# Performance work log

Hardware: AMD Instinct MI355X
Metric: run time of the kernel (lower is better)

The kernel has to match this reference:

```python
import jax, jax.numpy as jnp
import numpy as np

NUM_SKILLS = 300
EMB_SIZE = 256
CURVE_DIM = 64  # splits: 21 / 21 / 22
B, S = 512, 200


def setup_inputs() -> dict:
    key = jax.random.key(0)
    ks = jax.random.split(key, 11)
    d3 = CURVE_DIM // 3
    dm = d3 + CURVE_DIM % 3
    return {
        "q": jax.random.randint(ks[0], (B, S), 0, NUM_SKILLS, dtype=jnp.int32),
        "r": jax.random.randint(ks[1], (B, S), 0, 2, dtype=jnp.int32),
        "qry": jax.random.randint(ks[2], (B, S), 0, NUM_SKILLS, dtype=jnp.int32),
        "skill_w": jax.random.normal(ks[3], (d3,), jnp.float32),
        "skill_b": jax.random.normal(ks[4], (d3,), jnp.float32),
        "att_w": jax.random.normal(ks[5], (d3,), jnp.float32),
        "att_b": jax.random.normal(ks[6], (d3,), jnp.float32),
        "mast_w": jax.random.normal(ks[7], (dm,), jnp.float32),
        "mast_b": jax.random.normal(ks[8], (dm,), jnp.float32),
        "proj_w": jax.random.normal(ks[9], (EMB_SIZE, CURVE_DIM), jnp.float32) * 0.05,
        "proj_b": jax.random.normal(ks[10], (EMB_SIZE,), jnp.float32),
    }


def _running_counts(q, r):
    """Per-(b,t) running attempt count and correct count for the skill at (b,t).
    Returns attempts[B,S], correct[B,S] (float32), valid[B,S] (bool)."""
    b, s = q.shape
    rows = jnp.arange(b)
    valid = (q >= 0) & (q < NUM_SKILLS)
    idx = jnp.clip(q, 0, NUM_SKILLS - 1)

    def step(carry, xs):
        att, cor = carry  # [B, NUM_SKILLS] int32
        it, rt, vt = xs   # [B] each
        att = att.at[rows, it].add(vt.astype(jnp.int32))
        cor = cor.at[rows, it].add((rt * vt).astype(jnp.int32))
        return (att, cor), (att[rows, it], cor[rows, it])

    init = (jnp.zeros((b, NUM_SKILLS), jnp.int32), jnp.zeros((b, NUM_SKILLS), jnp.int32))
    xs = (idx.T, r.T, valid.T)  # scan over time
    _, (a_t, c_t) = jax.lax.scan(step, init, xs)
    return a_t.T.astype(jnp.float32), c_t.T.astype(jnp.float32), valid


def reference(q, r, qry, skill_w, skill_b, att_w, att_b, mast_w, mast_b, proj_w, proj_b):
    attempts, correct, valid = _running_counts(q, r)  # [B,S]
    mastery = correct / jnp.maximum(attempts, 1.0)
    skill_f = q.astype(jnp.float32)
    # Linear(1, d): scalar * w + b, broadcast over [B,S]
    s_enc = skill_f[..., None] * skill_w + skill_b        # [B,S,21]
    n_enc = attempts[..., None] * att_w + att_b           # [B,S,21]
    m_enc = mastery[..., None] * mast_w + mast_b          # [B,S,22]
    tup = jnp.concatenate([s_enc, n_enc, m_enc], axis=-1)  # [B,S,CURVE_DIM]
    traj = jnp.einsum('bsc,ec->bse', tup, proj_w) + proj_b  # [B,S,EMB]
    return jnp.where(valid[..., None], traj, 0.0)
```

## Files before the change

### kernel.cpp

```cpp
#include <hip/hip_runtime.h>

constexpr int NUM_SKILLS = 300;
constexpr int EMB = 256;
constexpr int CD  = 64;
constexpr int D3  = 21;
constexpr int DM  = 22;
constexpr int SEQ = 200;

__global__ __launch_bounds__(256)
void traj_enc_kernel(const int* __restrict__ q, const int* __restrict__ r,
                     const float* __restrict__ skill_w, const float* __restrict__ skill_b,
                     const float* __restrict__ att_w,   const float* __restrict__ att_b,
                     const float* __restrict__ mast_w,  const float* __restrict__ mast_b,
                     const float* __restrict__ proj_w,  const float* __restrict__ proj_b,
                     float* __restrict__ out)
{
    __shared__ __align__(16) float sA[EMB];
    __shared__ __align__(16) float sB[EMB];
    __shared__ __align__(16) float sC[EMB];
    __shared__ __align__(16) float sD[EMB];
    __shared__ float s_skill[SEQ], s_att[SEQ], s_mast[SEQ], s_valid[SEQ];
    __shared__ int   s_q[SEQ], s_r[SEQ];

    const int tid = threadIdx.x;
    const int b   = blockIdx.x;

    if (tid < SEQ) {
        s_q[tid] = q[b * SEQ + tid];
        s_r[tid] = r[b * SEQ + tid];
    }

    {
        const float* pw = proj_w + tid * CD;
        float ca = 0.f, cb = 0.f, cc = 0.f, cd = 0.f;
        #pragma unroll
        for (int i = 0; i < D3; ++i) { float w = pw[i];        ca = fmaf(w, skill_w[i], ca); cd = fmaf(w, skill_b[i], cd); }
        #pragma unroll
        for (int i = 0; i < D3; ++i) { float w = pw[D3 + i];   cb = fmaf(w, att_w[i],  cb);  cd = fmaf(w, att_b[i],  cd); }
        #pragma unroll
        for (int i = 0; i < DM; ++i) { float w = pw[2*D3 + i]; cc = fmaf(w, mast_w[i], cc);  cd = fmaf(w, mast_b[i], cd); }
        sA[tid] = ca; sB[tid] = cb; sC[tid] = cc; sD[tid] = cd + proj_b[tid];
    }
    __syncthreads();

    if (tid < SEQ) {
        const int myq = s_q[tid];
        int cnt = 0, cor = 0;
        for (int t = 0; t <= tid; ++t) {
            const int qt = s_q[t];
            const bool m = (qt >= 0) && (qt < NUM_SKILLS) && (qt == myq);
            if (m) { cnt += 1; cor += s_r[t]; }
        }
        const float att = (float)cnt;
        s_skill[tid] = (float)myq;
        s_att[tid]   = att;
        s_mast[tid]  = (float)cor / fmaxf(att, 1.0f);
        s_valid[tid] = (myq >= 0 && myq < NUM_SKILLS) ? 1.0f : 0.0f;
    }
    __syncthreads();

    const int e4   = tid & 63;
    const int ssub = tid >> 6;
    const float4 A4 = *reinterpret_cast<const float4*>(&sA[e4 * 4]);
    const float4 B4 = *reinterpret_cast<const float4*>(&sB[e4 * 4]);
    const float4 C4 = *reinterpret_cast<const float4*>(&sC[e4 * 4]);
    const float4 D4 = *reinterpret_cast<const float4*>(&sD[e4 * 4]);

    float4* __restrict__ out4 = reinterpret_cast<float4*>(out) + (size_t)b * SEQ * (EMB / 4);
    #pragma unroll 2
    for (int s0 = 0; s0 < SEQ; s0 += 4) {
        const int s = s0 + ssub;
        const float sk = s_skill[s];
        const float at = s_att[s];
        const float ma = s_mast[s];
        const float v  = s_valid[s];
        float4 o;
        o.x = v * fmaf(sk, A4.x, fmaf(at, B4.x, fmaf(ma, C4.x, D4.x)));
        o.y = v * fmaf(sk, A4.y, fmaf(at, B4.y, fmaf(ma, C4.y, D4.y)));
        o.z = v * fmaf(sk, A4.z, fmaf(at, B4.z, fmaf(ma, C4.z, D4.z)));
        o.w = v * fmaf(sk, A4.w, fmaf(at, B4.w, fmaf(ma, C4.w, D4.w)));
        out4[s * (EMB / 4) + e4] = o;
    }
}

extern "C" void kernel_launch(void* const* d_in, const int* in_sizes, int n_in,
                              void* d_out, int out_size, void* d_ws, size_t ws_size,
                              hipStream_t stream)
{
    const int* q        = (const int*)d_in[0];
    const int* r        = (const int*)d_in[1];
    const float* skill_w = (const float*)d_in[3];
    const float* skill_b = (const float*)d_in[4];
    const float* att_w   = (const float*)d_in[5];
    const float* att_b   = (const float*)d_in[6];
    const float* mast_w  = (const float*)d_in[7];
    const float* mast_b  = (const float*)d_in[8];
    const float* proj_w  = (const float*)d_in[9];
    const float* proj_b  = (const float*)d_in[10];
    float* out = (float*)d_out;

    const int B = in_sizes[0] / SEQ;
    traj_enc_kernel<<<B, 256, 0, stream>>>(q, r, skill_w, skill_b, att_w, att_b,
                                           mast_w, mast_b, proj_w, proj_b, out);
}
```

Measured before the change: 30.86 us.

## Split into prep and store kernels with coefficients computed once in workspace

Splits the fused kernel into two. A prep kernel computes the per-sequence running counts and writes packed float4 state to workspace, and only block 0 computes the projection coefficients. A store kernel then uses twice as many blocks to stream the large output from the state and coefficients. This removes the redundant per-block coefficient computation and serial prefix work from the store path, and the branchless inner count loop simplifies the prep. In exchange it adds a second launch and a round trip of state through global memory.

```diff
diff --git a/kernel.cpp b/kernel.cpp
--- a/kernel.cpp
+++ b/kernel.cpp
@@ -7,21 +7,17 @@
 constexpr int DM  = 22;
 constexpr int SEQ = 200;
 
+constexpr int COEF_FLOATS = 1024;
+
 __global__ __launch_bounds__(256)
-void traj_enc_kernel(const int* __restrict__ q, const int* __restrict__ r,
-                     const float* __restrict__ skill_w, const float* __restrict__ skill_b,
-                     const float* __restrict__ att_w,   const float* __restrict__ att_b,
-                     const float* __restrict__ mast_w,  const float* __restrict__ mast_b,
-                     const float* __restrict__ proj_w,  const float* __restrict__ proj_b,
-                     float* __restrict__ out)
+void traj_prep_kernel(const int* __restrict__ q, const int* __restrict__ r,
+                      const float* __restrict__ skill_w, const float* __restrict__ skill_b,
+                      const float* __restrict__ att_w,   const float* __restrict__ att_b,
+                      const float* __restrict__ mast_w,  const float* __restrict__ mast_b,
+                      const float* __restrict__ proj_w,  const float* __restrict__ proj_b,
+                      float* __restrict__ coef, float4* __restrict__ state)
 {
-    __shared__ __align__(16) float sA[EMB];
-    __shared__ __align__(16) float sB[EMB];
-    __shared__ __align__(16) float sC[EMB];
-    __shared__ __align__(16) float sD[EMB];
-    __shared__ float s_skill[SEQ], s_att[SEQ], s_mast[SEQ], s_valid[SEQ];
-    __shared__ int   s_q[SEQ], s_r[SEQ];
-
+    __shared__ int s_q[SEQ], s_r[SEQ];
     const int tid = threadIdx.x;
     const int b   = blockIdx.x;
 
@@ -30,7 +26,7 @@
         s_r[tid] = r[b * SEQ + tid];
     }
 
-    {
+    if (b == 0) {
         const float* pw = proj_w + tid * CD;
         float ca = 0.f, cb = 0.f, cc = 0.f, cd = 0.f;
         #pragma unroll
@@ -39,47 +35,62 @@
         for (int i = 0; i < D3; ++i) { float w = pw[D3 + i];   cb = fmaf(w, att_w[i],  cb);  cd = fmaf(w, att_b[i],  cd); }
         #pragma unroll
         for (int i = 0; i < DM; ++i) { float w = pw[2*D3 + i]; cc = fmaf(w, mast_w[i], cc);  cd = fmaf(w, mast_b[i], cd); }
-        sA[tid] = ca; sB[tid] = cb; sC[tid] = cc; sD[tid] = cd + proj_b[tid];
+        coef[tid]       = ca;
+        coef[256 + tid] = cb;
+        coef[512 + tid] = cc;
+        coef[768 + tid] = cd + proj_b[tid];
     }
     __syncthreads();
 
     if (tid < SEQ) {
         const int myq = s_q[tid];
+        const bool v  = (myq >= 0) && (myq < NUM_SKILLS);
         int cnt = 0, cor = 0;
         for (int t = 0; t <= tid; ++t) {
             const int qt = s_q[t];
-            const bool m = (qt >= 0) && (qt < NUM_SKILLS) && (qt == myq);
-            if (m) { cnt += 1; cor += s_r[t]; }
+            const bool m = (qt == myq) && v;
+            cnt += m ? 1 : 0;
+            cor += m ? s_r[t] : 0;
         }
         const float att = (float)cnt;
-        s_skill[tid] = (float)myq;
-        s_att[tid]   = att;
-        s_mast[tid]  = (float)cor / fmaxf(att, 1.0f);
-        s_valid[tid] = (myq >= 0 && myq < NUM_SKILLS) ? 1.0f : 0.0f;
+        float4 st;
+        st.x = (float)myq;
+        st.y = att;
+        st.z = (float)cor / fmaxf(att, 1.0f);
+        st.w = v ? 1.0f : 0.0f;
+        state[b * SEQ + tid] = st;
     }
-    __syncthreads();
+}
 
+__global__ __launch_bounds__(256)
+void traj_store_kernel(const float* __restrict__ coef, const float4* __restrict__ state,
+                       float4* __restrict__ out4)
+{
+    const int tid  = threadIdx.x;
     const int e4   = tid & 63;
     const int ssub = tid >> 6;
-    const float4 A4 = *reinterpret_cast<const float4*>(&sA[e4 * 4]);
-    const float4 B4 = *reinterpret_cast<const float4*>(&sB[e4 * 4]);
-    const float4 C4 = *reinterpret_cast<const float4*>(&sC[e4 * 4]);
-    const float4 D4 = *reinterpret_cast<const float4*>(&sD[e4 * 4]);
+    const int b      = blockIdx.x >> 1;
+    const int s_base = (blockIdx.x & 1) * (SEQ / 2);
 
-    float4* __restrict__ out4 = reinterpret_cast<float4*>(out) + (size_t)b * SEQ * (EMB / 4);
-    #pragma unroll 2
-    for (int s0 = 0; s0 < SEQ; s0 += 4) {
-        const int s = s0 + ssub;
-        const float sk = s_skill[s];
-        const float at = s_att[s];
-        const float ma = s_mast[s];
-        const float v  = s_valid[s];
-        float4 o;
-        o.x = v * fmaf(sk, A4.x, fmaf(at, B4.x, fmaf(ma, C4.x, D4.x)));
-        o.y = v * fmaf(sk, A4.y, fmaf(at, B4.y, fmaf(ma, C4.y, D4.y)));
-        o.z = v * fmaf(sk, A4.z, fmaf(at, B4.z, fmaf(ma, C4.z, D4.z)));
-        o.w = v * fmaf(sk, A4.w, fmaf(at, B4.w, fmaf(ma, C4.w, D4.w)));
-        out4[s * (EMB / 4) + e4] = o;
+    const float4* c4 = reinterpret_cast<const float4*>(coef);
+    const float4 A4 = c4[e4];
+    const float4 B4 = c4[64  + e4];
+    const float4 C4 = c4[128 + e4];
+    const float4 D4 = c4[192 + e4];
+
+    const float4* __restrict__ st = state + b * SEQ;
+    float4* __restrict__ o = out4 + (size_t)b * SEQ * (EMB / 4);
+
+    #pragma unroll 5
+    for (int s0 = 0; s0 < SEQ / 2; s0 += 4) {
+        const int s = s_base + s0 + ssub;
+        const float4 t = st[s];
+        float4 o4;
+        o4.x = t.w * fmaf(t.x, A4.x, fmaf(t.y, B4.x, fmaf(t.z, C4.x, D4.x)));
+        o4.y = t.w * fmaf(t.x, A4.y, fmaf(t.y, B4.y, fmaf(t.z, C4.y, D4.y)));
+        o4.z = t.w * fmaf(t.x, A4.z, fmaf(t.y, B4.z, fmaf(t.z, C4.z, D4.z)));
+        o4.w = t.w * fmaf(t.x, A4.w, fmaf(t.y, B4.w, fmaf(t.z, C4.w, D4.w)));
+        o[(size_t)s * (EMB / 4) + e4] = o4;
     }
 }
 
@@ -100,6 +111,12 @@
     float* out = (float*)d_out;
 
     const int B = in_sizes[0] / SEQ;
-    traj_enc_kernel<<<B, 256, 0, stream>>>(q, r, skill_w, skill_b, att_w, att_b,
-                                           mast_w, mast_b, proj_w, proj_b, out);
+
+    float*  coef  = (float*)d_ws;
+    float4* state = reinterpret_cast<float4*>((float*)d_ws + COEF_FLOATS);
+
+    traj_prep_kernel<<<B, 256, 0, stream>>>(q, r, skill_w, skill_b, att_w, att_b,
+                                            mast_w, mast_b, proj_w, proj_b, coef, state);
+    traj_store_kernel<<<B * 2, 256, 0, stream>>>(coef, state,
+                                                 reinterpret_cast<float4*>(out));
 }
```

Result: slower. 49.62 us (+60.8%).
